# Kernel tuning notes

Measured on AMD Instinct MI355X. Metric: run time of the kernel, lower is better.

## Reference

```python
import jax, jax.numpy as jnp
import numpy as np

N_NODES = 100000
N_EDGES = 1600000
IN_CH, HID_CH, OUT_CH = 128, 64, 32


def setup_inputs() -> dict:
    key = jax.random.key(0)
    k1, k2, k3, k4 = jax.random.split(key, 4)
    x = jax.random.normal(k1, (N_NODES, IN_CH), dtype=jnp.float32)
    edge_index = jax.random.randint(k2, (2, N_EDGES), 0, N_NODES, dtype=jnp.int32)
    # Glorot-ish scaling like PyG's GCNConv init
    W1 = jax.random.normal(k3, (IN_CH, HID_CH), dtype=jnp.float32) / np.sqrt(IN_CH)
    b1 = jnp.zeros((HID_CH,), dtype=jnp.float32)
    W2 = jax.random.normal(k4, (HID_CH, OUT_CH), dtype=jnp.float32) / np.sqrt(HID_CH)
    b2 = jnp.zeros((OUT_CH,), dtype=jnp.float32)
    return {"x": x, "edge_index": edge_index, "W1": W1, "b1": b1, "W2": W2, "b2": b2}


def reference(x, edge_index, W1, b1, W2, b2):
    # PyG GCNConv semantics: add self-loops, symmetric deg^{-1/2} normalization,
    # linear transform, scatter-add aggregation to destination nodes, add bias.
    N = x.shape[0]
    loops = jnp.arange(N, dtype=edge_index.dtype)
    src = jnp.concatenate([edge_index[0], loops])  # [E+N]
    dst = jnp.concatenate([edge_index[1], loops])  # [E+N]

    deg = jax.ops.segment_sum(jnp.ones_like(src, dtype=x.dtype), dst, num_segments=N)
    dis = jnp.where(deg > 0, jax.lax.rsqrt(jnp.maximum(deg, 1.0)), 0.0)  # deg^{-1/2}
    norm = (dis[src] * dis[dst])[:, None]  # [E+N, 1]

    def gcn_conv(h, W, b):
        h = h @ W                                   # [N, C_out]
        msgs = h[src] * norm                        # gather + scale, [E+N, C_out]
        return jax.ops.segment_sum(msgs, dst, num_segments=N) + b

    h = jax.nn.relu(gcn_conv(x, W1, b1))
    # dropout is identity in eval mode (training=False)
    return gcn_conv(h, W2, b2)
```

## Files before the change

kernel.cpp:

```cpp
#include <hip/hip_runtime.h>
#include <hip/hip_bf16.h>

#define IN_CH 128
#define HID_CH 64
#define OUT_CH 32
#define EPB 2048
#define MAXB 512

typedef unsigned short ushort_t;
typedef __attribute__((ext_vector_type(8))) short short8;
typedef __attribute__((ext_vector_type(4))) float float4v;

static __device__ __forceinline__ ushort_t f2bf(float f) {
    unsigned u = __float_as_uint(f);
    unsigned r = (u + 0x7fff + ((u >> 16) & 1)) >> 16;
    return (ushort_t)r;
}
static __device__ __forceinline__ float bf_lo(unsigned u) { return __uint_as_float(u << 16); }
static __device__ __forceinline__ float bf_hi(unsigned u) { return __uint_as_float(u & 0xffff0000u); }


__global__ __launch_bounds__(256) void k_partition(const int* __restrict__ src,
                                                   const int* __restrict__ dst,
                                                   int* __restrict__ gcursor,
                                                   unsigned* __restrict__ pairs,
                                                   int E, int nbk, int cap, int PB,
                                                   const float* __restrict__ W1,
                                                   unsigned* __restrict__ wsW) {
    __shared__ int lhist[MAXB];
    __shared__ int lbase[MAXB];
    __shared__ int lcur[MAXB];
    const int tid = threadIdx.x;

    if (blockIdx.x >= PB) {
        int s = (blockIdx.x - PB) * 256 + tid;
        int lane = s & 63;
        int nt = (s >> 6) & 3;
        int kc = s >> 8;
        int c = nt * 16 + (lane & 15);
        int k0 = kc * 32 + (lane >> 4) * 8;
        unsigned o[4];
#pragma unroll
        for (int d = 0; d < 4; ++d) {
            unsigned lo = f2bf(W1[(k0 + 2 * d) * 64 + c]);
            unsigned hi = f2bf(W1[(k0 + 2 * d + 1) * 64 + c]);
            o[d] = lo | (hi << 16);
        }
        ((uint4*)wsW)[s] = make_uint4(o[0], o[1], o[2], o[3]);
        return;
    }

    for (int b = tid; b < nbk; b += 256) { lhist[b] = 0; lcur[b] = 0; }
    __syncthreads();
    int s[8], d[8];
    const int e0 = blockIdx.x * EPB;
#pragma unroll
    for (int j = 0; j < 8; ++j) {
        int e = e0 + j * 256 + tid;
        if (e < E) {
            s[j] = src[e];
            d[j] = dst[e];
            atomicAdd(&lhist[d[j] >> 8], 1);
        } else {
            d[j] = -1;
        }
    }
    __syncthreads();
    for (int b = tid; b < nbk; b += 256)
        lbase[b] = lhist[b] ? atomicAdd(&gcursor[b], lhist[b]) : 0;
    __syncthreads();
#pragma unroll
    for (int j = 0; j < 8; ++j) {
        if (d[j] >= 0) {
            int b = d[j] >> 8;
            int loc = atomicAdd(&lcur[b], 1);
            int idx = lbase[b] + loc;
            if (idx < cap)
                pairs[(long long)b * cap + idx] = ((unsigned)s[j] << 8) | (unsigned)(d[j] & 255);
        }
    }
}


__global__ __launch_bounds__(256) void k_bucket_build(const unsigned* __restrict__ pairs,
                                                      const int* __restrict__ gcursor,
                                                      int* __restrict__ rowptr,
                                                      int* __restrict__ col,
                                                      float* __restrict__ dis,
                                                      unsigned* __restrict__ h1zero,
                                                      int cap, int N) {
    __shared__ int lc[256];
    __shared__ int ls[256];
    __shared__ int lcur[256];
    const int b = blockIdx.x, tid = threadIdx.x;

    if (b == 0 && tid < 32) h1zero[tid] = 0;

    int ga = min(gcursor[2 * tid], cap);
    int gb = min(gcursor[2 * tid + 1], cap);
    ls[tid] = ga + gb;
    __syncthreads();
    for (int off = 1; off < 256; off <<= 1) {
        int val = (tid >= off) ? ls[tid - off] : 0;
        __syncthreads();
        ls[tid] += val;
        __syncthreads();
    }
    const int p = b >> 1;
    const int base = (p ? ls[p - 1] : 0) + ((b & 1) ? min(gcursor[b - 1], cap) : 0);
    const int total = ls[255];
    __syncthreads();
    if (b == 0 && tid == 0) rowptr[N] = total;

    lc[tid] = 0;
    __syncthreads();
    const int cnt = min(gcursor[b], cap);
    const unsigned* pp = pairs + (long long)b * cap;
    for (int i = tid; i < cnt; i += 256) atomicAdd(&lc[pp[i] & 255], 1);
    __syncthreads();
    const int v = lc[tid];
    ls[tid] = v;
    __syncthreads();
    for (int off = 1; off < 256; off <<= 1) {
        int val = (tid >= off) ? ls[tid - off] : 0;
        __syncthreads();
        ls[tid] += val;
        __syncthreads();
    }
    const int excl = ls[tid] - v;
    const int row = b * 256 + tid;
    if (row < N) {
        rowptr[row] = base + excl;
        dis[row] = rsqrtf((float)(v + 1));
    }
    lcur[tid] = base + excl;
    __syncthreads();
    for (int i = tid; i < cnt; i += 256) {
        unsigned pk = pp[i];
        int pos = atomicAdd(&lcur[pk & 255], 1);
        col[pos] = (int)(pk >> 8);
    }
}


__global__ __launch_bounds__(256) void k_mm1(const float* __restrict__ X,
                                             const unsigned* __restrict__ wsW,
                                             const float* __restrict__ dis,
                                             ushort_t* __restrict__ H,
                                             unsigned* __restrict__ h2zero, int N) {
    const int tid = threadIdx.x;
    if (blockIdx.x == 0 && tid < 16) h2zero[tid] = 0;

    const int wv = tid >> 6, lane = tid & 63;
    const int quad = lane >> 4, n16 = lane & 15;
    const int rowbase = blockIdx.x * 64 + wv * 16;
    const int myrow = rowbase + n16;
    const bool rok = (myrow < N);

    float4v acc0 = {}, acc1 = {}, acc2 = {}, acc3 = {};

#pragma unroll
    for (int kc = 0; kc < 4; ++kc) {
        float4 xa = make_float4(0.f, 0.f, 0.f, 0.f), xb = xa;
        if (rok) {
            const float4* p = (const float4*)(X + (long long)myrow * 128 + kc * 32 + quad * 8);
            xa = p[0];
            xb = p[1];
        }
        unsigned pk[4];
        pk[0] = (unsigned)f2bf(xa.x) | ((unsigned)f2bf(xa.y) << 16);
        pk[1] = (unsigned)f2bf(xa.z) | ((unsigned)f2bf(xa.w) << 16);
        pk[2] = (unsigned)f2bf(xb.x) | ((unsigned)f2bf(xb.y) << 16);
        pk[3] = (unsigned)f2bf(xb.z) | ((unsigned)f2bf(xb.w) << 16);
        short8 a;
        a[0] = (short)(pk[0] & 0xffff); a[1] = (short)(pk[0] >> 16);
        a[2] = (short)(pk[1] & 0xffff); a[3] = (short)(pk[1] >> 16);
        a[4] = (short)(pk[2] & 0xffff); a[5] = (short)(pk[2] >> 16);
        a[6] = (short)(pk[3] & 0xffff); a[7] = (short)(pk[3] >> 16);

        const short8* wb = (const short8*)wsW;
        short8 b0 = wb[(kc * 4 + 0) * 64 + lane];
        short8 b1 = wb[(kc * 4 + 1) * 64 + lane];
        short8 b2 = wb[(kc * 4 + 2) * 64 + lane];
        short8 b3 = wb[(kc * 4 + 3) * 64 + lane];

        acc0 = __builtin_amdgcn_mfma_f32_16x16x32_bf16(a, b0, acc0, 0, 0, 0);
        acc1 = __builtin_amdgcn_mfma_f32_16x16x32_bf16(a, b1, acc1, 0, 0, 0);
        acc2 = __builtin_amdgcn_mfma_f32_16x16x32_bf16(a, b2, acc2, 0, 0, 0);
        acc3 = __builtin_amdgcn_mfma_f32_16x16x32_bf16(a, b3, acc3, 0, 0, 0);
    }

#pragma unroll
    for (int i = 0; i < 4; ++i) {
        int row = rowbase + quad * 4 + i;
        if (row < N) {
            float dr = dis[row];
            long long o = (long long)row * 64 + n16;
            H[o]      = f2bf(dr * acc0[i]);
            H[o + 16] = f2bf(dr * acc1[i]);
            H[o + 32] = f2bf(dr * acc2[i]);
            H[o + 48] = f2bf(dr * acc3[i]);
        }
    }
}


__global__ __launch_bounds__(256) void k_agg64_mm2(const unsigned* __restrict__ h,
                                                   const int* __restrict__ rowptr,
                                                   const int* __restrict__ col,
                                                   const float* __restrict__ dis,
                                                   const float* __restrict__ b1,
                                                   const float* __restrict__ W2,
                                                   unsigned* __restrict__ h2, int N) {
    __shared__ float zbuf[4][64];
    __shared__ float sW2[64 * 32];
    const int tid = threadIdx.x;
    for (int i = tid; i < 512; i += 256) ((float4*)sW2)[i] = ((const float4*)W2)[i];
    __syncthreads();

    const int wv = tid >> 6, lane = tid & 63;
    const int t = lane & 15, g = lane >> 4;
    const int c32 = lane & 31, kh = lane >> 5;
    const float4 bq = ((const float4*)b1)[t];

    const int wave0 = blockIdx.x * 4 + wv;
    const int nwaves = gridDim.x * 4;
    const uint2* h2w = (const uint2*)h;

    for (int row = wave0; row < N; row += nwaves) {
        const int start = rowptr[row];
        const int deg = rowptr[row + 1] - start;
        const float dr = dis[row];

        int myCol = N;
        if (lane < deg) myCol = col[start + lane];

        uint2 us = h2w[row * 16 + t];
        float a0 = 0.f, a1 = 0.f, a2 = 0.f, a3 = 0.f;
        if (g == 0) {
            a0 = bf_lo(us.x); a1 = bf_hi(us.x);
            a2 = bf_lo(us.y); a3 = bf_hi(us.y);
        }

        const int cnt = min(deg, 64);
        for (int k0 = 0; k0 < cnt; k0 += 32) {
#pragma unroll
            for (int u = 0; u < 8; ++u) {
                int slot = k0 + 4 * u + g;
                int s = __shfl(myCol, slot);
                uint2 uu = h2w[s * 16 + t];
                a0 += bf_lo(uu.x); a1 += bf_hi(uu.x);
                a2 += bf_lo(uu.y); a3 += bf_hi(uu.y);
            }
        }
        for (int j = start + 64 + g; j < start + deg; j += 4) {
            int s = col[j];
            uint2 uu = h2w[s * 16 + t];
            a0 += bf_lo(uu.x); a1 += bf_hi(uu.x);
            a2 += bf_lo(uu.y); a3 += bf_hi(uu.y);
        }
        a0 += __shfl_down(a0, 32); a1 += __shfl_down(a1, 32);
        a2 += __shfl_down(a2, 32); a3 += __shfl_down(a3, 32);
        a0 += __shfl_down(a0, 16); a1 += __shfl_down(a1, 16);
        a2 += __shfl_down(a2, 16); a3 += __shfl_down(a3, 16);

        if (lane < 16) {
            float4 zq;
            zq.x = bq.x + dr * a0;
            zq.y = bq.y + dr * a1;
            zq.z = bq.z + dr * a2;
            zq.w = bq.w + dr * a3;
            *(float4*)&zbuf[wv][4 * t] = zq;
        }
        __builtin_amdgcn_wave_barrier();

        float acc = 0.f;
        const float* zp = &zbuf[wv][kh * 32];
        const float* wp = &sW2[kh * 32 * 32 + c32];
#pragma unroll
        for (int k = 0; k < 32; k += 4) {
            float4 zv = *(const float4*)(zp + k);
            acc += fmaxf(zv.x, 0.f) * wp[k * 32] + fmaxf(zv.y, 0.f) * wp[(k + 1) * 32] +
                   fmaxf(zv.z, 0.f) * wp[(k + 2) * 32] + fmaxf(zv.w, 0.f) * wp[(k + 3) * 32];
        }
        __builtin_amdgcn_wave_barrier();
        acc += __shfl_down(acc, 32);

        const int tt = lane & 15;
        float o0 = __shfl(acc, 2 * tt);
        float o1 = __shfl(acc, 2 * tt + 1);
        if (lane < 16)
            h2[row * 16 + tt] = (unsigned)f2bf(dr * o0) | ((unsigned)f2bf(dr * o1) << 16);
    }
}


__global__ __launch_bounds__(256) void k_agg32(const unsigned* __restrict__ h,
                                               const int* __restrict__ rowptr,
                                               const int* __restrict__ col,
                                               const float* __restrict__ dis,
                                               const float* __restrict__ b,
                                               float* __restrict__ out, int N) {
    const int wave = (blockIdx.x * 256 + threadIdx.x) >> 6;
    const int lane = threadIdx.x & 63;
    if (wave >= N) return;
    const int row = wave;
    const int t = lane & 7, g = lane >> 3;

    const int start = rowptr[row];
    const int deg = rowptr[row + 1] - start;
    const float dr = dis[row];

    int myCol = N;
    if (lane < deg) myCol = col[start + lane];

    const uint2* hw = (const uint2*)h;
    uint2 us = hw[row * 8 + t];
    float a0 = 0.f, a1 = 0.f, a2 = 0.f, a3 = 0.f;
    if (g == 0) {
        a0 = bf_lo(us.x); a1 = bf_hi(us.x);
        a2 = bf_lo(us.y); a3 = bf_hi(us.y);
    }

    const int cnt = min(deg, 64);
    for (int k0 = 0; k0 < cnt; k0 += 64) {
#pragma unroll
        for (int u = 0; u < 8; ++u) {
            int slot = k0 + 8 * u + g;
            int s = __shfl(myCol, slot);
            uint2 uu = hw[s * 8 + t];
            a0 += bf_lo(uu.x); a1 += bf_hi(uu.x);
            a2 += bf_lo(uu.y); a3 += bf_hi(uu.y);
        }
    }
    for (int j = start + 64 + g; j < start + deg; j += 8) {
        int s = col[j];
        uint2 uu = hw[s * 8 + t];
        a0 += bf_lo(uu.x); a1 += bf_hi(uu.x);
        a2 += bf_lo(uu.y); a3 += bf_hi(uu.y);
    }
    a0 += __shfl_down(a0, 32); a1 += __shfl_down(a1, 32);
    a2 += __shfl_down(a2, 32); a3 += __shfl_down(a3, 32);
    a0 += __shfl_down(a0, 16); a1 += __shfl_down(a1, 16);
    a2 += __shfl_down(a2, 16); a3 += __shfl_down(a3, 16);
    a0 += __shfl_down(a0, 8);  a1 += __shfl_down(a1, 8);
    a2 += __shfl_down(a2, 8);  a3 += __shfl_down(a3, 8);

    if (lane < 8) {
        float4 bq = ((const float4*)b)[t];
        float4 o;
        o.x = bq.x + dr * a0;
        o.y = bq.y + dr * a1;
        o.z = bq.z + dr * a2;
        o.w = bq.w + dr * a3;
        ((float4*)out)[(long long)row * 8 + t] = o;
    }
}

extern "C" void kernel_launch(void* const* d_in, const int* in_sizes, int n_in,
                              void* d_out, int out_size, void* d_ws, size_t ws_size,
                              hipStream_t stream) {
    const float* x  = (const float*)d_in[0];
    const int*   ei = (const int*)d_in[1];
    const float* W1 = (const float*)d_in[2];
    const float* b1 = (const float*)d_in[3];
    const float* W2 = (const float*)d_in[4];
    const float* b2 = (const float*)d_in[5];
    float* out = (float*)d_out;

    const int N = in_sizes[0] / IN_CH;
    const int E = in_sizes[1] / 2;
    const int* esrc = ei;
    const int* edst = ei + E;

    int nbk = (N + 255) >> 8;
    if (nbk > MAXB) nbk = MAXB;
    const int per_b = (E + nbk - 1) / nbk;
    const int cap = per_b + per_b / 4 + 256;

    int* rowptr   = (int*)d_ws;
    int* gcursor  = rowptr + (((N + 1) + 15) & ~15);
    unsigned* wsW = (unsigned*)(gcursor + MAXB);
    int* col      = (int*)(wsW + 4096);
    float* dis    = (float*)(col + ((E + 15) & ~15));
    ushort_t* h1  = (ushort_t*)(dis + ((N + 15) & ~15));
    unsigned* scratch = (unsigned*)(h1 + (((long long)(N + 1) * 64 + 31) & ~31LL));
    unsigned* pairs = scratch;
    unsigned* h2    = scratch;

    const int B = 256;
    const int PB = (E + EPB - 1) / EPB;

    hipMemsetAsync(gcursor, 0, MAXB * sizeof(int), stream);
    k_partition<<<PB + 4, B, 0, stream>>>(esrc, edst, gcursor, pairs, E, nbk, cap, PB, W1, wsW);
    k_bucket_build<<<nbk, B, 0, stream>>>(pairs, gcursor, rowptr, col, dis,
                                          (unsigned*)(h1 + (long long)N * 64), cap, N);

    k_mm1<<<(N + 63) / 64, B, 0, stream>>>(x, wsW, dis, h1, h2 + (long long)N * 16, N);

    const int fblocks = (N + 31) / 32;
    k_agg64_mm2<<<fblocks, B, 0, stream>>>((const unsigned*)h1, rowptr, col, dis, b1, W2, h2, N);

    k_agg32<<<(int)(((long long)N * 64 + B - 1) / B), B, 0, stream>>>((const unsigned*)h2, rowptr, col, dis, b2, out, N);
}
```

Before: 247.4 us.

## Use f16 MFMA for second linear layer and trim gather unrolling

```diff
diff --git a/kernel.cpp b/kernel.cpp
--- a/kernel.cpp
+++ b/kernel.cpp
@@ -10,6 +10,7 @@
 typedef unsigned short ushort_t;
 typedef __attribute__((ext_vector_type(8))) short short8;
 typedef __attribute__((ext_vector_type(4))) float float4v;
+using half8 = __attribute__((ext_vector_type(8))) _Float16;
 
 static __device__ __forceinline__ ushort_t f2bf(float f) {
     unsigned u = __float_as_uint(f);
@@ -18,6 +19,19 @@
 }
 static __device__ __forceinline__ float bf_lo(unsigned u) { return __uint_as_float(u << 16); }
 static __device__ __forceinline__ float bf_hi(unsigned u) { return __uint_as_float(u & 0xffff0000u); }
+
+static __device__ __forceinline__ unsigned f2h2(float lo, float hi) {
+    union { _Float16 h[2]; unsigned u; } v;
+    v.h[0] = (_Float16)lo;
+    v.h[1] = (_Float16)hi;
+    return v.u;
+}
+static __device__ __forceinline__ unsigned pkh(float a, float b) {
+    auto p = __builtin_amdgcn_cvt_pkrtz(a, b);
+    union { decltype(p) h; unsigned u; } v;
+    v.h = p;
+    return v.u;
+}
 
 
 __global__ __launch_bounds__(256) void k_partition(const int* __restrict__ src,
@@ -26,6 +40,7 @@
                                                    unsigned* __restrict__ pairs,
                                                    int E, int nbk, int cap, int PB,
                                                    const float* __restrict__ W1,
+                                                   const float* __restrict__ W2,
                                                    unsigned* __restrict__ wsW) {
     __shared__ int lhist[MAXB];
     __shared__ int lbase[MAXB];
@@ -34,19 +49,32 @@
 
     if (blockIdx.x >= PB) {
         int s = (blockIdx.x - PB) * 256 + tid;
-        int lane = s & 63;
-        int nt = (s >> 6) & 3;
-        int kc = s >> 8;
-        int c = nt * 16 + (lane & 15);
-        int k0 = kc * 32 + (lane >> 4) * 8;
-        unsigned o[4];
-#pragma unroll
-        for (int d = 0; d < 4; ++d) {
-            unsigned lo = f2bf(W1[(k0 + 2 * d) * 64 + c]);
-            unsigned hi = f2bf(W1[(k0 + 2 * d + 1) * 64 + c]);
-            o[d] = lo | (hi << 16);
-        }
-        ((uint4*)wsW)[s] = make_uint4(o[0], o[1], o[2], o[3]);
+        if (s < 1024) {
+            int lane = s & 63;
+            int nt = (s >> 6) & 3;
+            int kc = s >> 8;
+            int c = nt * 16 + (lane & 15);
+            int k0 = kc * 32 + (lane >> 4) * 8;
+            unsigned o[4];
+#pragma unroll
+            for (int d = 0; d < 4; ++d) {
+                unsigned lo = f2bf(W1[(k0 + 2 * d) * 64 + c]);
+                unsigned hi = f2bf(W1[(k0 + 2 * d + 1) * 64 + c]);
+                o[d] = lo | (hi << 16);
+            }
+            ((uint4*)wsW)[s] = make_uint4(o[0], o[1], o[2], o[3]);
+        } else {
+            int q = s - 1024;
+            int lane = q & 63;
+            int f = q >> 6;
+            int c = (f & 1) * 16 + (lane & 15);
+            int k0 = (f >> 1) * 32 + (lane >> 4) * 8;
+            unsigned o[4];
+#pragma unroll
+            for (int d = 0; d < 4; ++d)
+                o[d] = f2h2(W2[(k0 + 2 * d) * 32 + c], W2[(k0 + 2 * d + 1) * 32 + c]);
+            ((uint4*)wsW)[1024 + q] = make_uint4(o[0], o[1], o[2], o[3]);
+        }
         return;
     }
 
@@ -205,27 +233,30 @@
 }
 
 
-__global__ __launch_bounds__(256) void k_agg64_mm2(const unsigned* __restrict__ h,
-                                                   const int* __restrict__ rowptr,
-                                                   const int* __restrict__ col,
-                                                   const float* __restrict__ dis,
-                                                   const float* __restrict__ b1,
-                                                   const float* __restrict__ W2,
-                                                   unsigned* __restrict__ h2, int N) {
-    __shared__ float zbuf[4][64];
-    __shared__ float sW2[64 * 32];
+__global__ __launch_bounds__(256, 8) void k_agg64_mm2(const unsigned* __restrict__ h,
+                                                      const int* __restrict__ rowptr,
+                                                      const int* __restrict__ col,
+                                                      const float* __restrict__ dis,
+                                                      const float* __restrict__ b1,
+                                                      const unsigned* __restrict__ wsW2,
+                                                      unsigned* __restrict__ h2, int N) {
+    __shared__ __align__(16) _Float16 zbl[4][64];
     const int tid = threadIdx.x;
-    for (int i = tid; i < 512; i += 256) ((float4*)sW2)[i] = ((const float4*)W2)[i];
-    __syncthreads();
-
     const int wv = tid >> 6, lane = tid & 63;
     const int t = lane & 15, g = lane >> 4;
-    const int c32 = lane & 31, kh = lane >> 5;
+    const int q8 = g * 8;
     const float4 bq = ((const float4*)b1)[t];
 
+    const half8* wfh = (const half8*)wsW2;
+    const half8 bf00 = wfh[lane];
+    const half8 bf01 = wfh[64 + lane];
+    const half8 bf10 = wfh[128 + lane];
+    const half8 bf11 = wfh[192 + lane];
+
+    ushort_t* H2u = (ushort_t*)h2;
+    const uint2* h2w = (const uint2*)h;
     const int wave0 = blockIdx.x * 4 + wv;
     const int nwaves = gridDim.x * 4;
-    const uint2* h2w = (const uint2*)h;
 
     for (int row = wave0; row < N; row += nwaves) {
         const int start = rowptr[row];
@@ -236,61 +267,65 @@
         if (lane < deg) myCol = col[start + lane];
 
         uint2 us = h2w[row * 16 + t];
-        float a0 = 0.f, a1 = 0.f, a2 = 0.f, a3 = 0.f;
+        float2 a01 = make_float2(0.f, 0.f), a23 = make_float2(0.f, 0.f);
         if (g == 0) {
-            a0 = bf_lo(us.x); a1 = bf_hi(us.x);
-            a2 = bf_lo(us.y); a3 = bf_hi(us.y);
-        }
-
+            a01 = make_float2(bf_lo(us.x), bf_hi(us.x));
+            a23 = make_float2(bf_lo(us.y), bf_hi(us.y));
+        }
+
+#define GAT64(SLOT)                                                   \
+    {                                                                 \
+        int s_ = __shfl(myCol, (SLOT));                               \
+        uint2 uu = h2w[s_ * 16 + t];                                  \
+        a01 += make_float2(bf_lo(uu.x), bf_hi(uu.x));                 \
+        a23 += make_float2(bf_lo(uu.y), bf_hi(uu.y));                 \
+    }
         const int cnt = min(deg, 64);
         for (int k0 = 0; k0 < cnt; k0 += 32) {
-#pragma unroll
-            for (int u = 0; u < 8; ++u) {
-                int slot = k0 + 4 * u + g;
-                int s = __shfl(myCol, slot);
-                uint2 uu = h2w[s * 16 + t];
-                a0 += bf_lo(uu.x); a1 += bf_hi(uu.x);
-                a2 += bf_lo(uu.y); a3 += bf_hi(uu.y);
+            if (cnt - k0 > 16) {
+#pragma unroll
+                for (int u = 0; u < 8; ++u) GAT64(k0 + 4 * u + g)
+            } else {
+#pragma unroll
+                for (int u = 0; u < 4; ++u) GAT64(k0 + 4 * u + g)
             }
         }
         for (int j = start + 64 + g; j < start + deg; j += 4) {
-            int s = col[j];
-            uint2 uu = h2w[s * 16 + t];
-            a0 += bf_lo(uu.x); a1 += bf_hi(uu.x);
-            a2 += bf_lo(uu.y); a3 += bf_hi(uu.y);
-        }
-        a0 += __shfl_down(a0, 32); a1 += __shfl_down(a1, 32);
-        a2 += __shfl_down(a2, 32); a3 += __shfl_down(a3, 32);
-        a0 += __shfl_down(a0, 16); a1 += __shfl_down(a1, 16);
-        a2 += __shfl_down(a2, 16); a3 += __shfl_down(a3, 16);
+            int s_ = col[j];
+            uint2 uu = h2w[s_ * 16 + t];
+            a01 += make_float2(bf_lo(uu.x), bf_hi(uu.x));
+            a23 += make_float2(bf_lo(uu.y), bf_hi(uu.y));
+        }
+#undef GAT64
+
+        float A0 = a01.x, A1 = a01.y, A2 = a23.x, A3 = a23.y;
+        A0 += __shfl_down(A0, 32); A1 += __shfl_down(A1, 32);
+        A2 += __shfl_down(A2, 32); A3 += __shfl_down(A3, 32);
+        A0 += __shfl_down(A0, 16); A1 += __shfl_down(A1, 16);
+        A2 += __shfl_down(A2, 16); A3 += __shfl_down(A3, 16);
 
         if (lane < 16) {
-            float4 zq;
-            zq.x = bq.x + dr * a0;
-            zq.y = bq.y + dr * a1;
-            zq.z = bq.z + dr * a2;
-            zq.w = bq.w + dr * a3;
-            *(float4*)&zbuf[wv][4 * t] = zq;
+            float z0 = fmaxf(fmaf(dr, A0, bq.x), 0.f);
+            float z1 = fmaxf(fmaf(dr, A1, bq.y), 0.f);
+            float z2 = fmaxf(fmaf(dr, A2, bq.z), 0.f);
+            float z3 = fmaxf(fmaf(dr, A3, bq.w), 0.f);
+            *(uint2*)&zbl[wv][4 * t] = make_uint2(pkh(z0, z1), pkh(z2, z3));
         }
         __builtin_amdgcn_wave_barrier();
 
-        float acc = 0.f;
-        const float* zp = &zbuf[wv][kh * 32];
-        const float* wp = &sW2[kh * 32 * 32 + c32];
-#pragma unroll
-        for (int k = 0; k < 32; k += 4) {
-            float4 zv = *(const float4*)(zp + k);
-            acc += fmaxf(zv.x, 0.f) * wp[k * 32] + fmaxf(zv.y, 0.f) * wp[(k + 1) * 32] +
-                   fmaxf(zv.z, 0.f) * wp[(k + 2) * 32] + fmaxf(zv.w, 0.f) * wp[(k + 3) * 32];
-        }
+        half8 af0 = *(const half8*)&zbl[wv][q8];
+        half8 af1 = *(const half8*)&zbl[wv][q8 + 32];
+
+        float4v c0 = {};
+        c0 = __builtin_amdgcn_mfma_f32_16x16x32_f16(af0, bf00, c0, 0, 0, 0);
+        c0 = __builtin_amdgcn_mfma_f32_16x16x32_f16(af1, bf10, c0, 0, 0, 0);
+        float4v c1 = {};
+        c1 = __builtin_amdgcn_mfma_f32_16x16x32_f16(af0, bf01, c1, 0, 0, 0);
+        c1 = __builtin_amdgcn_mfma_f32_16x16x32_f16(af1, bf11, c1, 0, 0, 0);
         __builtin_amdgcn_wave_barrier();
-        acc += __shfl_down(acc, 32);
-
-        const int tt = lane & 15;
-        float o0 = __shfl(acc, 2 * tt);
-        float o1 = __shfl(acc, 2 * tt + 1);
-        if (lane < 16)
-            h2[row * 16 + tt] = (unsigned)f2bf(dr * o0) | ((unsigned)f2bf(dr * o1) << 16);
+
+        float v = (lane < 16) ? c0[0] : c1[0];
+        if (lane < 32) H2u[row * 32 + lane] = f2bf(dr * v);
     }
 }
 
@@ -316,43 +351,53 @@
 
     const uint2* hw = (const uint2*)h;
     uint2 us = hw[row * 8 + t];
-    float a0 = 0.f, a1 = 0.f, a2 = 0.f, a3 = 0.f;
+    float2 a01 = make_float2(0.f, 0.f), a23 = make_float2(0.f, 0.f);
     if (g == 0) {
-        a0 = bf_lo(us.x); a1 = bf_hi(us.x);
-        a2 = bf_lo(us.y); a3 = bf_hi(us.y);
-    }
-
+        a01 = make_float2(bf_lo(us.x), bf_hi(us.x));
+        a23 = make_float2(bf_lo(us.y), bf_hi(us.y));
+    }
+
+#define GAT32(SLOT)                                                   \
+    {                                                                 \
+        int s_ = __shfl(myCol, (SLOT));                               \
+        uint2 uu = hw[s_ * 8 + t];                                    \
+        a01 += make_float2(bf_lo(uu.x), bf_hi(uu.x));                 \
+        a23 += make_float2(bf_lo(uu.y), bf_hi(uu.y));                 \
+    }
     const int cnt = min(deg, 64);
-    for (int k0 = 0; k0 < cnt; k0 += 64) {
-#pragma unroll
-        for (int u = 0; u < 8; ++u) {
-            int slot = k0 + 8 * u + g;
-            int s = __shfl(myCol, slot);
-            uint2 uu = hw[s * 8 + t];
-            a0 += bf_lo(uu.x); a1 += bf_hi(uu.x);
-            a2 += bf_lo(uu.y); a3 += bf_hi(uu.y);
-        }
+    if (cnt > 32) {
+#pragma unroll
+        for (int u = 0; u < 8; ++u) GAT32(8 * u + g)
+    } else if (cnt > 16) {
+#pragma unroll
+        for (int u = 0; u < 4; ++u) GAT32(8 * u + g)
+    } else {
+#pragma unroll
+        for (int u = 0; u < 2; ++u) GAT32(8 * u + g)
     }
     for (int j = start + 64 + g; j < start + deg; j += 8) {
-        int s = col[j];
-        uint2 uu = hw[s * 8 + t];
-        a0 += bf_lo(uu.x); a1 += bf_hi(uu.x);
-        a2 += bf_lo(uu.y); a3 += bf_hi(uu.y);
-    }
-    a0 += __shfl_down(a0, 32); a1 += __shfl_down(a1, 32);
-    a2 += __shfl_down(a2, 32); a3 += __shfl_down(a3, 32);
-    a0 += __shfl_down(a0, 16); a1 += __shfl_down(a1, 16);
-    a2 += __shfl_down(a2, 16); a3 += __shfl_down(a3, 16);
-    a0 += __shfl_down(a0, 8);  a1 += __shfl_down(a1, 8);
-    a2 += __shfl_down(a2, 8);  a3 += __shfl_down(a3, 8);
+        int s_ = col[j];
+        uint2 uu = hw[s_ * 8 + t];
+        a01 += make_float2(bf_lo(uu.x), bf_hi(uu.x));
+        a23 += make_float2(bf_lo(uu.y), bf_hi(uu.y));
+    }
+#undef GAT32
+
+    float A0 = a01.x, A1 = a01.y, A2 = a23.x, A3 = a23.y;
+    A0 += __shfl_down(A0, 32); A1 += __shfl_down(A1, 32);
+    A2 += __shfl_down(A2, 32); A3 += __shfl_down(A3, 32);
+    A0 += __shfl_down(A0, 16); A1 += __shfl_down(A1, 16);
+    A2 += __shfl_down(A2, 16); A3 += __shfl_down(A3, 16);
+    A0 += __shfl_down(A0, 8);  A1 += __shfl_down(A1, 8);
+    A2 += __shfl_down(A2, 8);  A3 += __shfl_down(A3, 8);
 
     if (lane < 8) {
         float4 bq = ((const float4*)b)[t];
         float4 o;
-        o.x = bq.x + dr * a0;
-        o.y = bq.y + dr * a1;
-        o.z = bq.z + dr * a2;
-        o.w = bq.w + dr * a3;
+        o.x = bq.x + dr * A0;
+        o.y = bq.y + dr * A1;
+        o.z = bq.z + dr * A2;
+        o.w = bq.w + dr * A3;
         ((float4*)out)[(long long)row * 8 + t] = o;
     }
 }
@@ -381,7 +426,7 @@
     int* rowptr   = (int*)d_ws;
     int* gcursor  = rowptr + (((N + 1) + 15) & ~15);
     unsigned* wsW = (unsigned*)(gcursor + MAXB);
-    int* col      = (int*)(wsW + 4096);
+    int* col      = (int*)(wsW + 5120);
     float* dis    = (float*)(col + ((E + 15) & ~15));
     ushort_t* h1  = (ushort_t*)(dis + ((N + 15) & ~15));
     unsigned* scratch = (unsigned*)(h1 + (((long long)(N + 1) * 64 + 31) & ~31LL));
@@ -392,14 +437,14 @@
     const int PB = (E + EPB - 1) / EPB;
 
     hipMemsetAsync(gcursor, 0, MAXB * sizeof(int), stream);
-    k_partition<<<PB + 4, B, 0, stream>>>(esrc, edst, gcursor, pairs, E, nbk, cap, PB, W1, wsW);
+    k_partition<<<PB + 5, B, 0, stream>>>(esrc, edst, gcursor, pairs, E, nbk, cap, PB, W1, W2, wsW);
     k_bucket_build<<<nbk, B, 0, stream>>>(pairs, gcursor, rowptr, col, dis,
                                           (unsigned*)(h1 + (long long)N * 64), cap, N);
 
     k_mm1<<<(N + 63) / 64, B, 0, stream>>>(x, wsW, dis, h1, h2 + (long long)N * 16, N);
 
-    const int fblocks = (N + 31) / 32;
-    k_agg64_mm2<<<fblocks, B, 0, stream>>>((const unsigned*)h1, rowptr, col, dis, b1, W2, h2, N);
+    k_agg64_mm2<<<2048, B, 0, stream>>>((const unsigned*)h1, rowptr, col, dis, b1,
+                                        wsW + 4096, h2, N);
 
     k_agg32<<<(int)(((long long)N * 64 + B - 1) / B), B, 0, stream>>>((const unsigned*)h2, rowptr, col, dis, b2, out, N);
 }
```

New measurement: 244.9 us. About the same (-1.0%).
